# Kernel optimization log

Hardware: AMD Instinct MI355X
Metric: run time of the kernel (lower is better)

Reference implementation:

```python
import jax, jax.numpy as jnp
import numpy as np

LABEL_SMOOTHING = 0.1


def setup_inputs() -> dict:
    key = jax.random.key(0)
    k1, k2, k3 = jax.random.split(key, 3)
    B, N, D = 16384, 1000, 1000  # code structurally requires D == n_classes == N
    inputs = jax.random.uniform(k1, (B, D), dtype=jnp.float32)
    labels = jax.random.randint(k2, (B,), 0, N, dtype=jnp.int64)
    code_book = jax.random.uniform(k3, (N, D), dtype=jnp.float32)
    return {"inputs": inputs, "labels": labels, "code_book": code_book}


def reference(inputs, labels, code_book):
    # inputs: [B, D], code_book: [N, D], D == N (n_classes)
    n_classes = inputs.shape[1]
    # soft targets with label smoothing (same as scatter_ + smoothing)
    soft_target = jax.nn.one_hot(labels, n_classes, dtype=inputs.dtype)
    soft_target = soft_target * (1.0 - LABEL_SMOOTHING) + LABEL_SMOOTHING / n_classes
    # Hamming similarity: sum_d [o*c + (1-o)*(1-c)]  ==  o@c.T + (1-o)@(1-c).T
    # (algebraic rewrite of the [B, N, D] broadcast in the original; same math)
    similarity = (jnp.einsum("bd,nd->bn", inputs, code_book)
                  + jnp.einsum("bd,nd->bn", 1.0 - inputs, 1.0 - code_book))
    logp = jax.nn.log_softmax(similarity, axis=1)
    return jnp.mean(jnp.sum(-soft_target * logp, axis=1))
```

## Files before the change

### kernel.cpp

```cpp
#include <hip/hip_runtime.h>

typedef __attribute__((ext_vector_type(8))) short bf16x8;
typedef __attribute__((ext_vector_type(4))) float f32x4;

#define AS1 __attribute__((address_space(1)))
#define AS3 __attribute__((address_space(3)))

__device__ static inline void gl2lds16(const void* g, void* l) {
  __builtin_amdgcn_global_load_lds((const AS1 unsigned int*)g, (AS3 unsigned int*)l, 16, 0, 0);
}

__device__ static inline unsigned short f2bf(float x) {
  unsigned int u = __float_as_uint(x);
  unsigned int r = u + 0x7FFFu + ((u >> 16) & 1u);
  return (unsigned short)(r >> 16);
}

__global__ __launch_bounds__(256) void prep_all_k(
    const float* __restrict__ in, const int* __restrict__ labraw,
    const float* __restrict__ cb, unsigned short* __restrict__ a,
    unsigned short* __restrict__ b, float* __restrict__ rowsum,
    int* __restrict__ labs, float* __restrict__ lin, float* __restrict__ out) {
  const int bx = blockIdx.x, t = threadIdx.x;
  if (bx < 8192) {
    int idx = bx * 256 + t;
    int row = idx >> 7, g = idx & 127;
    union { unsigned short u[8]; uint4 v; } pk;
    if (g < 125) {
      const float4* p = (const float4*)(in + (size_t)row * 1000 + g * 8);
      float4 v0 = p[0], v1 = p[1];
      pk.u[0] = f2bf(2.f * v0.x); pk.u[1] = f2bf(2.f * v0.y);
      pk.u[2] = f2bf(2.f * v0.z); pk.u[3] = f2bf(2.f * v0.w);
      pk.u[4] = f2bf(2.f * v1.x); pk.u[5] = f2bf(2.f * v1.y);
      pk.u[6] = f2bf(2.f * v1.z); pk.u[7] = f2bf(2.f * v1.w);
    } else {
      pk.v = make_uint4(0, 0, 0, 0);
    }
    *(uint4*)(a + ((size_t)row << 10) + (g << 3)) = pk.v;
  } else if (bx < 9216) {
    int n = bx - 8192;
    float s = 0.f;
#pragma unroll
    for (int j = 0; j < 4; ++j) {
      int c = t + j * 256;
      float v = 0.f;
      if (n < 1000 && c < 1000) v = cb[(size_t)n * 1000 + c];
      s += v;
      b[((size_t)n << 10) + c] = f2bf(v);
    }
    __shared__ float red[256];
    red[t] = s;
    __syncthreads();
    for (int o = 128; o > 0; o >>= 1) {
      if (t < o) red[t] += red[t + o];
      __syncthreads();
    }
    if (t == 0) rowsum[n] = (n < 1000) ? red[0] : 0.f;
  } else {
    __shared__ int nz;
    if (t == 0) nz = 0;
    __syncthreads();
    if (labraw[2 * t + 1] != 0) atomicAdd(&nz, 1);
    __syncthreads();
    bool is64 = (nz < 32);
    int row = (bx - 9216) * 256 + t;
    labs[row] = is64 ? labraw[2 * row] : labraw[row];
    if (bx == 9216 && t == 0) { lin[0] = 0.f; out[0] = 0.f; }
  }
}

__global__ __launch_bounds__(512, 2) void coding_loss_k(
    const unsigned short* __restrict__ Ag,
    const unsigned short* __restrict__ Bg,
    const float* __restrict__ rowsum,
    const int* __restrict__ labels,
    float* __restrict__ Z,
    float* __restrict__ lin) {
  extern __shared__ __align__(16) unsigned short lds[];

  const int t    = threadIdx.x;
  const int lane = t & 63;
  const int w    = t >> 6;
  const int wr   = w >> 2;
  const int wc   = w & 3;
  const int g16  = lane >> 4;
  const int c16  = lane & 15;
  const int ct   = blockIdx.x & 3;
  const int rt   = blockIdx.x >> 2;
  const int r0   = rt << 8;
  const int c0   = ct << 8;

  size_t a_src[2], b_src[2]; int dstoff[2];
#pragma unroll
  for (int i = 0; i < 2; ++i) {
    int ch = i * 512 + t, row = ch >> 2;
    int sg = (ch & 3) ^ ((row >> 1) & 3);
    a_src[i] = (size_t)(r0 + row) * 1024 + sg * 8;
    b_src[i] = (size_t)(c0 + row) * 1024 + sg * 8;
    dstoff[i] = ch * 8;
  }
  int a_eoff[8], b_eoff[4];
#pragma unroll
  for (int i = 0; i < 8; ++i) {
    int ar = wr * 128 + i * 16 + c16;
    a_eoff[i] = ar * 32 + ((g16 ^ ((ar >> 1) & 3)) << 3);
  }
#pragma unroll
  for (int i = 0; i < 4; ++i) {
    int br = wc * 64 + i * 16 + c16;
    b_eoff[i] = br * 32 + ((g16 ^ ((br >> 1) & 3)) << 3);
  }

  f32x4 acc[8][4];
#pragma unroll
  for (int mi = 0; mi < 8; ++mi)
#pragma unroll
    for (int ni = 0; ni < 4; ++ni) acc[mi][ni] = (f32x4)(0.f);

#define TILE(J, DO_STAGE, DO_WAIT, WAIT_IMM)                                    \
  {                                                                             \
    unsigned short* pa = lds + ((J) & 3) * 8192;                                \
    unsigned short* pb = lds + 32768 + ((J) & 3) * 8192;                        \
    unsigned short* sa = lds + (((J) + 3) & 3) * 8192;                          \
    unsigned short* sb = lds + 32768 + (((J) + 3) & 3) * 8192;                  \
    if (DO_STAGE) {                                                             \
      _Pragma("unroll") for (int i = 0; i < 2; ++i)                             \
          gl2lds16(Ag + a_src[i] + ((J) + 3) * 32, sa + dstoff[i]);             \
      _Pragma("unroll") for (int i = 0; i < 2; ++i)                             \
          gl2lds16(Bg + b_src[i] + ((J) + 3) * 32, sb + dstoff[i]);             \
    }                                                                           \
    bf16x8 af[4], af2[4], bv[4];                                                \
    _Pragma("unroll") for (int i = 0; i < 4; ++i)                               \
        af[i] = *(const bf16x8*)(pa + a_eoff[i]);                               \
    _Pragma("unroll") for (int i = 0; i < 4; ++i)                               \
        bv[i] = *(const bf16x8*)(pb + b_eoff[i]);                               \
    _Pragma("unroll") for (int i = 0; i < 4; ++i)                               \
        af2[i] = *(const bf16x8*)(pa + a_eoff[i + 4]);                          \
    __builtin_amdgcn_s_setprio(1);                                              \
    _Pragma("unroll") for (int mi = 0; mi < 4; ++mi)                            \
      _Pragma("unroll") for (int ni = 0; ni < 4; ++ni)                          \
        acc[mi][ni] =                                                           \
            __builtin_amdgcn_mfma_f32_16x16x32_bf16(af[mi], bv[ni], acc[mi][ni], 0, 0, 0); \
    _Pragma("unroll") for (int mi = 0; mi < 4; ++mi)                            \
      _Pragma("unroll") for (int ni = 0; ni < 4; ++ni)                          \
        acc[mi + 4][ni] =                                                       \
            __builtin_amdgcn_mfma_f32_16x16x32_bf16(af2[mi], bv[ni], acc[mi + 4][ni], 0, 0, 0); \
    __builtin_amdgcn_s_setprio(0);                                              \
    if (DO_WAIT) __builtin_amdgcn_s_waitcnt(WAIT_IMM);                          \
    __builtin_amdgcn_s_barrier();                                               \
    __builtin_amdgcn_sched_barrier(0);                                          \
  }

#pragma unroll
  for (int q = 0; q < 3; ++q) {
#pragma unroll
    for (int i = 0; i < 2; ++i)
      gl2lds16(Ag + a_src[i] + q * 32, lds + q * 8192 + dstoff[i]);
#pragma unroll
    for (int i = 0; i < 2; ++i)
      gl2lds16(Bg + b_src[i] + q * 32, lds + 32768 + q * 8192 + dstoff[i]);
  }
  __builtin_amdgcn_s_waitcnt(0xF78);
  __builtin_amdgcn_s_barrier();
  __builtin_amdgcn_sched_barrier(0);

#pragma unroll 4
  for (int J = 0; J < 28; ++J) TILE(J, 1, 1, 0xF78);
  TILE(28, 1, 1, 0xF78);
  TILE(29, 0, 1, 0xF74);
  TILE(30, 0, 1, 0xF70);
  TILE(31, 0, 0, 0xF70);
#undef TILE
  __syncthreads();

  float* zbuf = (float*)lds;
  float* lbuf = zbuf + 1024;
  float rs[4]; int gcol[4];
#pragma unroll
  for (int ni = 0; ni < 4; ++ni) {
    gcol[ni] = c0 + wc * 64 + ni * 16 + c16;
    rs[ni]   = rowsum[gcol[ni]];
  }
  float lacc = 0.f;
#pragma unroll
  for (int mi = 0; mi < 8; ++mi) {
#pragma unroll
    for (int r = 0; r < 4; ++r) {
      int lrow = mi * 16 + g16 * 4 + r;
      int labv = labels[r0 + wr * 128 + lrow];
      float e = 0.f;
#pragma unroll
      for (int ni = 0; ni < 4; ++ni) {
        float S = acc[mi][ni][r] - rs[ni];
        e += __expf(S - 40.f);
        lacc += 1e-4f * S;
        if (gcol[ni] == labv) lacc += 0.9f * S;
      }
      e += __shfl_xor(e, 1, 64);
      e += __shfl_xor(e, 2, 64);
      e += __shfl_xor(e, 4, 64);
      e += __shfl_xor(e, 8, 64);
      if (c16 == 0) zbuf[w * 128 + lrow] = e;
    }
  }
#pragma unroll
  for (int d = 1; d < 64; d <<= 1) lacc += __shfl_xor(lacc, d, 64);
  if (lane == 0) lbuf[w] = lacc;
  __syncthreads();
  if (t < 256) {
    int wrg = t >> 7, l7 = t & 127;
    float z = zbuf[(wrg * 4 + 0) * 128 + l7] + zbuf[(wrg * 4 + 1) * 128 + l7] +
              zbuf[(wrg * 4 + 2) * 128 + l7] + zbuf[(wrg * 4 + 3) * 128 + l7];
    Z[ct * 16384 + r0 + t] = z;
  }
  if (t == 0)
    atomicAdd(lin, lbuf[0] + lbuf[1] + lbuf[2] + lbuf[3] +
                   lbuf[4] + lbuf[5] + lbuf[6] + lbuf[7]);
}

__global__ __launch_bounds__(256) void finalize_k(const float* __restrict__ Z,
                                                  const float* __restrict__ lin,
                                                  float* __restrict__ out) {
  int t = threadIdx.x;
  int row = blockIdx.x * 256 + t;
  float v = 40.f + logf(Z[row] + Z[16384 + row] + Z[2 * 16384 + row] + Z[3 * 16384 + row]);
#pragma unroll
  for (int d = 1; d < 64; d <<= 1) v += __shfl_xor(v, d, 64);
  __shared__ float s[4];
  if ((t & 63) == 0) s[t >> 6] = v;
  __syncthreads();
  if (t == 0) {
    float tot = s[0] + s[1] + s[2] + s[3];
    if (blockIdx.x == 0) tot -= lin[0];
    atomicAdd(out, tot * (1.f / 16384.f));
  }
}

extern "C" void kernel_launch(void* const* d_in, const int* in_sizes, int n_in,
                              void* d_out, int out_size, void* d_ws, size_t ws_size,
                              hipStream_t stream) {
  const float* inputs = (const float*)d_in[0];
  const int* labraw   = (const int*)d_in[1];
  const float* code   = (const float*)d_in[2];

  unsigned short* a_bf = (unsigned short*)d_ws;
  unsigned short* b_bf = a_bf + (size_t)16384 * 1024;
  float* rowsum        = (float*)(b_bf + (size_t)1024 * 1024);
  float* Z             = rowsum + 1024;
  float* lin           = Z + 4 * 16384;
  int* labs            = (int*)(lin + 1);

  static int lds_attr_set = 0;
  if (!lds_attr_set) {
    hipFuncSetAttribute(reinterpret_cast<const void*>(coding_loss_k),
                        hipFuncAttributeMaxDynamicSharedMemorySize, 131072);
    lds_attr_set = 1;
  }

  prep_all_k<<<9280, 256, 0, stream>>>(inputs, labraw, code, a_bf, b_bf, rowsum,
                                       labs, lin, (float*)d_out);
  coding_loss_k<<<256, 512, 131072, stream>>>(a_bf, b_bf, rowsum, labs, Z, lin);
  finalize_k<<<64, 256, 0, stream>>>(Z, lin, (float*)d_out);
}
```

Baseline: 140.5 us.

## Fuse fp32-to-bf16 input conversion into GEMM main loop with register staging

The separate prep pass that converted the 16384x1000 fp32 inputs to padded bf16 in workspace is removed. The GEMM kernel now loads fp32 rows straight from the inputs, converts them in registers and writes bf16 into a double-buffered static LDS tile. This drops a full write and reread of the converted A matrix. In exchange the previous 4-stage async global-to-LDS pipeline becomes a 2-stage register-prefetch pipeline with a full __syncthreads per tile, and each block reads twice as many bytes for A (fp32) and repeats the conversion work.

```diff
diff --git a/kernel.cpp b/kernel.cpp
--- a/kernel.cpp
+++ b/kernel.cpp
@@ -16,29 +16,13 @@
   return (unsigned short)(r >> 16);
 }
 
-__global__ __launch_bounds__(256) void prep_all_k(
-    const float* __restrict__ in, const int* __restrict__ labraw,
-    const float* __restrict__ cb, unsigned short* __restrict__ a,
+__global__ __launch_bounds__(256) void prep_bl_k(
+    const float* __restrict__ cb, const int* __restrict__ labraw,
     unsigned short* __restrict__ b, float* __restrict__ rowsum,
     int* __restrict__ labs, float* __restrict__ lin, float* __restrict__ out) {
   const int bx = blockIdx.x, t = threadIdx.x;
-  if (bx < 8192) {
-    int idx = bx * 256 + t;
-    int row = idx >> 7, g = idx & 127;
-    union { unsigned short u[8]; uint4 v; } pk;
-    if (g < 125) {
-      const float4* p = (const float4*)(in + (size_t)row * 1000 + g * 8);
-      float4 v0 = p[0], v1 = p[1];
-      pk.u[0] = f2bf(2.f * v0.x); pk.u[1] = f2bf(2.f * v0.y);
-      pk.u[2] = f2bf(2.f * v0.z); pk.u[3] = f2bf(2.f * v0.w);
-      pk.u[4] = f2bf(2.f * v1.x); pk.u[5] = f2bf(2.f * v1.y);
-      pk.u[6] = f2bf(2.f * v1.z); pk.u[7] = f2bf(2.f * v1.w);
-    } else {
-      pk.v = make_uint4(0, 0, 0, 0);
-    }
-    *(uint4*)(a + ((size_t)row << 10) + (g << 3)) = pk.v;
-  } else if (bx < 9216) {
-    int n = bx - 8192;
+  if (bx < 1024) {
+    int n = bx;
     float s = 0.f;
 #pragma unroll
     for (int j = 0; j < 4; ++j) {
@@ -63,20 +47,20 @@
     if (labraw[2 * t + 1] != 0) atomicAdd(&nz, 1);
     __syncthreads();
     bool is64 = (nz < 32);
-    int row = (bx - 9216) * 256 + t;
+    int row = (bx - 1024) * 256 + t;
     labs[row] = is64 ? labraw[2 * row] : labraw[row];
-    if (bx == 9216 && t == 0) { lin[0] = 0.f; out[0] = 0.f; }
+    if (bx == 1024 && t == 0) { lin[0] = 0.f; out[0] = 0.f; }
   }
 }
 
 __global__ __launch_bounds__(512, 2) void coding_loss_k(
-    const unsigned short* __restrict__ Ag,
+    const float* __restrict__ In,
     const unsigned short* __restrict__ Bg,
     const float* __restrict__ rowsum,
     const int* __restrict__ labels,
     float* __restrict__ Z,
     float* __restrict__ lin) {
-  extern __shared__ __align__(16) unsigned short lds[];
+  __shared__ __align__(16) unsigned short lds[32768];
 
   const int t    = threadIdx.x;
   const int lane = t & 63;
@@ -90,14 +74,17 @@
   const int r0   = rt << 8;
   const int c0   = ct << 8;
 
-  size_t a_src[2], b_src[2]; int dstoff[2];
+  const int sg  = (t & 3) ^ ((t >> 3) & 3);
+  const int rA0 = t >> 2, rA1 = 128 + (t >> 2);
+  const float* pA0 = In + (size_t)(r0 + rA0) * 1000 + sg * 8;
+  const float* pA1 = In + (size_t)(r0 + rA1) * 1000 + sg * 8;
+  size_t b_src[2]; int bdst[2];
 #pragma unroll
   for (int i = 0; i < 2; ++i) {
     int ch = i * 512 + t, row = ch >> 2;
-    int sg = (ch & 3) ^ ((row >> 1) & 3);
-    a_src[i] = (size_t)(r0 + row) * 1024 + sg * 8;
-    b_src[i] = (size_t)(c0 + row) * 1024 + sg * 8;
-    dstoff[i] = ch * 8;
+    int sgb = (ch & 3) ^ ((row >> 1) & 3);
+    b_src[i] = (size_t)(c0 + row) * 1024 + sgb * 8;
+    bdst[i] = ch * 8;
   }
   int a_eoff[8], b_eoff[4];
 #pragma unroll
@@ -117,60 +104,73 @@
 #pragma unroll
     for (int ni = 0; ni < 4; ++ni) acc[mi][ni] = (f32x4)(0.f);
 
-#define TILE(J, DO_STAGE, DO_WAIT, WAIT_IMM)                                    \
-  {                                                                             \
-    unsigned short* pa = lds + ((J) & 3) * 8192;                                \
-    unsigned short* pb = lds + 32768 + ((J) & 3) * 8192;                        \
-    unsigned short* sa = lds + (((J) + 3) & 3) * 8192;                          \
-    unsigned short* sb = lds + 32768 + (((J) + 3) & 3) * 8192;                  \
-    if (DO_STAGE) {                                                             \
-      _Pragma("unroll") for (int i = 0; i < 2; ++i)                             \
-          gl2lds16(Ag + a_src[i] + ((J) + 3) * 32, sa + dstoff[i]);             \
-      _Pragma("unroll") for (int i = 0; i < 2; ++i)                             \
-          gl2lds16(Bg + b_src[i] + ((J) + 3) * 32, sb + dstoff[i]);             \
-    }                                                                           \
-    bf16x8 af[4], af2[4], bv[4];                                                \
-    _Pragma("unroll") for (int i = 0; i < 4; ++i)                               \
-        af[i] = *(const bf16x8*)(pa + a_eoff[i]);                               \
-    _Pragma("unroll") for (int i = 0; i < 4; ++i)                               \
-        bv[i] = *(const bf16x8*)(pb + b_eoff[i]);                               \
-    _Pragma("unroll") for (int i = 0; i < 4; ++i)                               \
-        af2[i] = *(const bf16x8*)(pa + a_eoff[i + 4]);                          \
-    __builtin_amdgcn_s_setprio(1);                                              \
-    _Pragma("unroll") for (int mi = 0; mi < 4; ++mi)                            \
-      _Pragma("unroll") for (int ni = 0; ni < 4; ++ni)                          \
-        acc[mi][ni] =                                                           \
+#define LOADA(js, G0A, G0B, G1A, G1B)                                          \
+  {                                                                            \
+    if ((js) < 31 || sg == 0) {                                                \
+      const float4* q0 = (const float4*)(pA0 + (js) * 32);                     \
+      const float4* q1 = (const float4*)(pA1 + (js) * 32);                     \
+      G0A = q0[0]; G0B = q0[1]; G1A = q1[0]; G1B = q1[1];                      \
+    } else {                                                                   \
+      G0A = G0B = G1A = G1B = make_float4(0.f, 0.f, 0.f, 0.f);                 \
+    }                                                                          \
+  }
+
+#define CVWRA(p, G0A, G0B, G1A, G1B)                                           \
+  {                                                                            \
+    union { unsigned short u[8]; uint4 v; } w0, w1;                            \
+    w0.u[0] = f2bf(2.f * G0A.x); w0.u[1] = f2bf(2.f * G0A.y);                  \
+    w0.u[2] = f2bf(2.f * G0A.z); w0.u[3] = f2bf(2.f * G0A.w);                  \
+    w0.u[4] = f2bf(2.f * G0B.x); w0.u[5] = f2bf(2.f * G0B.y);                  \
+    w0.u[6] = f2bf(2.f * G0B.z); w0.u[7] = f2bf(2.f * G0B.w);                  \
+    w1.u[0] = f2bf(2.f * G1A.x); w1.u[1] = f2bf(2.f * G1A.y);                  \
+    w1.u[2] = f2bf(2.f * G1A.z); w1.u[3] = f2bf(2.f * G1A.w);                  \
+    w1.u[4] = f2bf(2.f * G1B.x); w1.u[5] = f2bf(2.f * G1B.y);                  \
+    w1.u[6] = f2bf(2.f * G1B.z); w1.u[7] = f2bf(2.f * G1B.w);                  \
+    *(uint4*)(lds + ((p) << 13) + t * 8) = w0.v;                               \
+    *(uint4*)(lds + ((p) << 13) + 4096 + t * 8) = w1.v;                        \
+  }
+
+#define COMPUTE(p)                                                             \
+  {                                                                            \
+    const unsigned short* pa = lds + ((p) << 13);                              \
+    const unsigned short* pb = lds + 16384 + ((p) << 13);                      \
+    bf16x8 af[4], af2[4], bv[4];                                               \
+    _Pragma("unroll") for (int i = 0; i < 4; ++i)                              \
+        af[i] = *(const bf16x8*)(pa + a_eoff[i]);                              \
+    _Pragma("unroll") for (int i = 0; i < 4; ++i)                              \
+        bv[i] = *(const bf16x8*)(pb + b_eoff[i]);                              \
+    _Pragma("unroll") for (int i = 0; i < 4; ++i)                              \
+        af2[i] = *(const bf16x8*)(pa + a_eoff[i + 4]);                         \
+    _Pragma("unroll") for (int mi = 0; mi < 4; ++mi)                           \
+      _Pragma("unroll") for (int ni = 0; ni < 4; ++ni)                         \
+        acc[mi][ni] =                                                          \
             __builtin_amdgcn_mfma_f32_16x16x32_bf16(af[mi], bv[ni], acc[mi][ni], 0, 0, 0); \
-    _Pragma("unroll") for (int mi = 0; mi < 4; ++mi)                            \
-      _Pragma("unroll") for (int ni = 0; ni < 4; ++ni)                          \
-        acc[mi + 4][ni] =                                                       \
+    _Pragma("unroll") for (int mi = 0; mi < 4; ++mi)                           \
+      _Pragma("unroll") for (int ni = 0; ni < 4; ++ni)                         \
+        acc[mi + 4][ni] =                                                      \
             __builtin_amdgcn_mfma_f32_16x16x32_bf16(af2[mi], bv[ni], acc[mi + 4][ni], 0, 0, 0); \
-    __builtin_amdgcn_s_setprio(0);                                              \
-    if (DO_WAIT) __builtin_amdgcn_s_waitcnt(WAIT_IMM);                          \
-    __builtin_amdgcn_s_barrier();                                               \
-    __builtin_amdgcn_sched_barrier(0);                                          \
-  }
-
-#pragma unroll
-  for (int q = 0; q < 3; ++q) {
-#pragma unroll
-    for (int i = 0; i < 2; ++i)
-      gl2lds16(Ag + a_src[i] + q * 32, lds + q * 8192 + dstoff[i]);
-#pragma unroll
-    for (int i = 0; i < 2; ++i)
-      gl2lds16(Bg + b_src[i] + q * 32, lds + 32768 + q * 8192 + dstoff[i]);
-  }
-  __builtin_amdgcn_s_waitcnt(0xF78);
-  __builtin_amdgcn_s_barrier();
-  __builtin_amdgcn_sched_barrier(0);
-
-#pragma unroll 4
-  for (int J = 0; J < 28; ++J) TILE(J, 1, 1, 0xF78);
-  TILE(28, 1, 1, 0xF78);
-  TILE(29, 0, 1, 0xF74);
-  TILE(30, 0, 1, 0xF70);
-  TILE(31, 0, 0, 0xF70);
-#undef TILE
+  }
+
+  {
+    float4 g0a, g0b, g1a, g1b;
+    LOADA(0, g0a, g0b, g1a, g1b);
+    gl2lds16(Bg + b_src[0], lds + 16384 + bdst[0]);
+    gl2lds16(Bg + b_src[1], lds + 16384 + bdst[1]);
+    CVWRA(0, g0a, g0b, g1a, g1b);
+    __syncthreads();
+  }
+
+  for (int J = 0; J < 31; ++J) {
+    const int jn = J + 1;
+    float4 g0a, g0b, g1a, g1b;
+    LOADA(jn, g0a, g0b, g1a, g1b);
+    gl2lds16(Bg + b_src[0] + jn * 32, lds + 16384 + ((jn & 1) << 13) + bdst[0]);
+    gl2lds16(Bg + b_src[1] + jn * 32, lds + 16384 + ((jn & 1) << 13) + bdst[1]);
+    COMPUTE(J & 1);
+    CVWRA(jn & 1, g0a, g0b, g1a, g1b);
+    __syncthreads();
+  }
+  COMPUTE(1);
   __syncthreads();
 
   float* zbuf = (float*)lds;
@@ -216,6 +216,9 @@
   if (t == 0)
     atomicAdd(lin, lbuf[0] + lbuf[1] + lbuf[2] + lbuf[3] +
                    lbuf[4] + lbuf[5] + lbuf[6] + lbuf[7]);
+#undef LOADA
+#undef CVWRA
+#undef COMPUTE
 }
 
 __global__ __launch_bounds__(256) void finalize_k(const float* __restrict__ Z,
@@ -243,22 +246,14 @@
   const int* labraw   = (const int*)d_in[1];
   const float* code   = (const float*)d_in[2];
 
-  unsigned short* a_bf = (unsigned short*)d_ws;
-  unsigned short* b_bf = a_bf + (size_t)16384 * 1024;
+  unsigned short* b_bf = (unsigned short*)d_ws;
   float* rowsum        = (float*)(b_bf + (size_t)1024 * 1024);
   float* Z             = rowsum + 1024;
   float* lin           = Z + 4 * 16384;
   int* labs            = (int*)(lin + 1);
 
-  static int lds_attr_set = 0;
-  if (!lds_attr_set) {
-    hipFuncSetAttribute(reinterpret_cast<const void*>(coding_loss_k),
-                        hipFuncAttributeMaxDynamicSharedMemorySize, 131072);
-    lds_attr_set = 1;
-  }
-
-  prep_all_k<<<9280, 256, 0, stream>>>(inputs, labraw, code, a_bf, b_bf, rowsum,
-                                       labs, lin, (float*)d_out);
-  coding_loss_k<<<256, 512, 131072, stream>>>(a_bf, b_bf, rowsum, labs, Z, lin);
+  prep_bl_k<<<1088, 256, 0, stream>>>(code, labraw, b_bf, rowsum, labs, lin,
+                                      (float*)d_out);
+  coding_loss_k<<<256, 512, 0, stream>>>(inputs, b_bf, rowsum, labs, Z, lin);
   finalize_k<<<64, 256, 0, stream>>>(Z, lin, (float*)d_out);
 }
```

New measurement: 166.9 us. 18.8% more time.

## Shrink GEMM block tile, use triple-buffered pipeline, fuse finalize via last-block reduction

Applied to the files above, without the earlier changes.

The GEMM kernel moves from 256x256 tiles with 512 threads and a 4-stage LDS ring to 128x256 tiles with 256 threads and a 3-stage ring. This doubles the grid to 512 blocks, and block IDs are remapped so neighbouring blocks are spread across XCDs. The separate finalize kernel is removed: a global counter lets the last block perform the logsumexp reduction and write the output, which saves a launch. In exchange, A-tile reuse per block is lower and the final reduction runs serially in a single block.

```diff
diff --git a/kernel.cpp b/kernel.cpp
--- a/kernel.cpp
+++ b/kernel.cpp
@@ -20,7 +20,8 @@
     const float* __restrict__ in, const int* __restrict__ labraw,
     const float* __restrict__ cb, unsigned short* __restrict__ a,
     unsigned short* __restrict__ b, float* __restrict__ rowsum,
-    int* __restrict__ labs, float* __restrict__ lin, float* __restrict__ out) {
+    int* __restrict__ labs, float* __restrict__ lin, float* __restrict__ out,
+    int* __restrict__ cnt) {
   const int bx = blockIdx.x, t = threadIdx.x;
   if (bx < 8192) {
     int idx = bx * 256 + t;
@@ -65,49 +66,56 @@
     bool is64 = (nz < 32);
     int row = (bx - 9216) * 256 + t;
     labs[row] = is64 ? labraw[2 * row] : labraw[row];
-    if (bx == 9216 && t == 0) { lin[0] = 0.f; out[0] = 0.f; }
-  }
-}
-
-__global__ __launch_bounds__(512, 2) void coding_loss_k(
+    if (bx == 9216 && t == 0) { lin[0] = 0.f; out[0] = 0.f; cnt[0] = 0; }
+  }
+}
+
+__global__ __launch_bounds__(256, 2) void coding_loss_k(
     const unsigned short* __restrict__ Ag,
     const unsigned short* __restrict__ Bg,
     const float* __restrict__ rowsum,
     const int* __restrict__ labels,
     float* __restrict__ Z,
-    float* __restrict__ lin) {
+    float* __restrict__ lin,
+    float* __restrict__ out,
+    int* __restrict__ cnt) {
   extern __shared__ __align__(16) unsigned short lds[];
 
   const int t    = threadIdx.x;
   const int lane = t & 63;
   const int w    = t >> 6;
-  const int wr   = w >> 2;
-  const int wc   = w & 3;
   const int g16  = lane >> 4;
   const int c16  = lane & 15;
-  const int ct   = blockIdx.x & 3;
-  const int rt   = blockIdx.x >> 2;
-  const int r0   = rt << 8;
+  const int bid  = blockIdx.x;
+  const int L    = ((bid & 7) << 6) | (bid >> 3);
+  const int ct   = L & 3;
+  const int rt   = L >> 2;
+  const int r0   = rt << 7;
   const int c0   = ct << 8;
 
-  size_t a_src[2], b_src[2]; int dstoff[2];
+  const int sg = (t & 3) ^ ((t >> 3) & 3);
+  const int rA = t >> 2;
+  size_t a_src[2]; int adst[2];
 #pragma unroll
   for (int i = 0; i < 2; ++i) {
-    int ch = i * 512 + t, row = ch >> 2;
-    int sg = (ch & 3) ^ ((row >> 1) & 3);
-    a_src[i] = (size_t)(r0 + row) * 1024 + sg * 8;
-    b_src[i] = (size_t)(c0 + row) * 1024 + sg * 8;
-    dstoff[i] = ch * 8;
+    a_src[i] = (size_t)(r0 + rA + 64 * i) * 1024 + sg * 8;
+    adst[i] = (t + 256 * i) * 8;
+  }
+  size_t b_src[4]; int bdst[4];
+#pragma unroll
+  for (int i = 0; i < 4; ++i) {
+    b_src[i] = (size_t)(c0 + rA + 64 * i) * 1024 + sg * 8;
+    bdst[i] = (t + 256 * i) * 8;
   }
   int a_eoff[8], b_eoff[4];
 #pragma unroll
   for (int i = 0; i < 8; ++i) {
-    int ar = wr * 128 + i * 16 + c16;
+    int ar = i * 16 + c16;
     a_eoff[i] = ar * 32 + ((g16 ^ ((ar >> 1) & 3)) << 3);
   }
 #pragma unroll
   for (int i = 0; i < 4; ++i) {
-    int br = wc * 64 + i * 16 + c16;
+    int br = w * 64 + i * 16 + c16;
     b_eoff[i] = br * 32 + ((g16 ^ ((br >> 1) & 3)) << 3);
   }
 
@@ -117,68 +125,74 @@
 #pragma unroll
     for (int ni = 0; ni < 4; ++ni) acc[mi][ni] = (f32x4)(0.f);
 
-#define TILE(J, DO_STAGE, DO_WAIT, WAIT_IMM)                                    \
-  {                                                                             \
-    unsigned short* pa = lds + ((J) & 3) * 8192;                                \
-    unsigned short* pb = lds + 32768 + ((J) & 3) * 8192;                        \
-    unsigned short* sa = lds + (((J) + 3) & 3) * 8192;                          \
-    unsigned short* sb = lds + 32768 + (((J) + 3) & 3) * 8192;                  \
-    if (DO_STAGE) {                                                             \
-      _Pragma("unroll") for (int i = 0; i < 2; ++i)                             \
-          gl2lds16(Ag + a_src[i] + ((J) + 3) * 32, sa + dstoff[i]);             \
-      _Pragma("unroll") for (int i = 0; i < 2; ++i)                             \
-          gl2lds16(Bg + b_src[i] + ((J) + 3) * 32, sb + dstoff[i]);             \
-    }                                                                           \
-    bf16x8 af[4], af2[4], bv[4];                                                \
-    _Pragma("unroll") for (int i = 0; i < 4; ++i)                               \
-        af[i] = *(const bf16x8*)(pa + a_eoff[i]);                               \
-    _Pragma("unroll") for (int i = 0; i < 4; ++i)                               \
-        bv[i] = *(const bf16x8*)(pb + b_eoff[i]);                               \
-    _Pragma("unroll") for (int i = 0; i < 4; ++i)                               \
-        af2[i] = *(const bf16x8*)(pa + a_eoff[i + 4]);                          \
-    __builtin_amdgcn_s_setprio(1);                                              \
-    _Pragma("unroll") for (int mi = 0; mi < 4; ++mi)                            \
-      _Pragma("unroll") for (int ni = 0; ni < 4; ++ni)                          \
-        acc[mi][ni] =                                                           \
+#define STAGE(js, qa, qb)                                                      \
+  {                                                                            \
+    _Pragma("unroll") for (int i = 0; i < 2; ++i)                              \
+        gl2lds16(Ag + a_src[i] + (size_t)(js) * 32, lds + (qa)*4096 + adst[i]); \
+    _Pragma("unroll") for (int i = 0; i < 4; ++i)                              \
+        gl2lds16(Bg + b_src[i] + (size_t)(js) * 32,                            \
+                 lds + 12288 + (qb)*8192 + bdst[i]);                           \
+  }
+
+#define COMPUTE(q)                                                             \
+  {                                                                            \
+    const unsigned short* pa = lds + (q)*4096;                                 \
+    const unsigned short* pb = lds + 12288 + (q)*8192;                         \
+    bf16x8 af[4], af2[4], bv[4];                                               \
+    _Pragma("unroll") for (int i = 0; i < 4; ++i)                              \
+        af[i] = *(const bf16x8*)(pa + a_eoff[i]);                              \
+    _Pragma("unroll") for (int i = 0; i < 4; ++i)                              \
+        bv[i] = *(const bf16x8*)(pb + b_eoff[i]);                              \
+    _Pragma("unroll") for (int i = 0; i < 4; ++i)                              \
+        af2[i] = *(const bf16x8*)(pa + a_eoff[i + 4]);                         \
+    _Pragma("unroll") for (int mi = 0; mi < 4; ++mi)                           \
+      _Pragma("unroll") for (int ni = 0; ni < 4; ++ni)                         \
+        acc[mi][ni] =                                                          \
             __builtin_amdgcn_mfma_f32_16x16x32_bf16(af[mi], bv[ni], acc[mi][ni], 0, 0, 0); \
-    _Pragma("unroll") for (int mi = 0; mi < 4; ++mi)                            \
-      _Pragma("unroll") for (int ni = 0; ni < 4; ++ni)                          \
-        acc[mi + 4][ni] =                                                       \
+    _Pragma("unroll") for (int mi = 0; mi < 4; ++mi)                           \
+      _Pragma("unroll") for (int ni = 0; ni < 4; ++ni)                         \
+        acc[mi + 4][ni] =                                                      \
             __builtin_amdgcn_mfma_f32_16x16x32_bf16(af2[mi], bv[ni], acc[mi + 4][ni], 0, 0, 0); \
-    __builtin_amdgcn_s_setprio(0);                                              \
-    if (DO_WAIT) __builtin_amdgcn_s_waitcnt(WAIT_IMM);                          \
-    __builtin_amdgcn_s_barrier();                                               \
-    __builtin_amdgcn_sched_barrier(0);                                          \
-  }
-
-#pragma unroll
-  for (int q = 0; q < 3; ++q) {
-#pragma unroll
-    for (int i = 0; i < 2; ++i)
-      gl2lds16(Ag + a_src[i] + q * 32, lds + q * 8192 + dstoff[i]);
-#pragma unroll
-    for (int i = 0; i < 2; ++i)
-      gl2lds16(Bg + b_src[i] + q * 32, lds + 32768 + q * 8192 + dstoff[i]);
-  }
-  __builtin_amdgcn_s_waitcnt(0xF78);
+  }
+
+#define REGION(q, js)                                                          \
+  {                                                                            \
+    STAGE(js, (q + 2) % 3, (q + 2) % 3);                                       \
+    COMPUTE(q);                                                                \
+    __builtin_amdgcn_sched_barrier(0);                                         \
+    __builtin_amdgcn_s_waitcnt(0xF76);                           \
+    __builtin_amdgcn_s_barrier();                                              \
+    __builtin_amdgcn_sched_barrier(0);                                         \
+  }
+
+  STAGE(0, 0, 0);
+  STAGE(1, 1, 1);
+  __builtin_amdgcn_s_waitcnt(0xF76);
   __builtin_amdgcn_s_barrier();
   __builtin_amdgcn_sched_barrier(0);
 
-#pragma unroll 4
-  for (int J = 0; J < 28; ++J) TILE(J, 1, 1, 0xF78);
-  TILE(28, 1, 1, 0xF78);
-  TILE(29, 0, 1, 0xF74);
-  TILE(30, 0, 1, 0xF70);
-  TILE(31, 0, 0, 0xF70);
-#undef TILE
+  for (int j0 = 0; j0 < 30; j0 += 3) {
+    REGION(0, j0 + 2);
+    REGION(1, j0 + 3);
+    REGION(2, j0 + 4);
+  }
+  COMPUTE(0);
+  __builtin_amdgcn_sched_barrier(0);
+  __builtin_amdgcn_s_waitcnt(0xF70);
+  __builtin_amdgcn_s_barrier();
+  __builtin_amdgcn_sched_barrier(0);
+  COMPUTE(1);
   __syncthreads();
+#undef STAGE
+#undef COMPUTE
+#undef REGION
 
   float* zbuf = (float*)lds;
-  float* lbuf = zbuf + 1024;
+  float* lbuf = zbuf + 512;
   float rs[4]; int gcol[4];
 #pragma unroll
   for (int ni = 0; ni < 4; ++ni) {
-    gcol[ni] = c0 + wc * 64 + ni * 16 + c16;
+    gcol[ni] = c0 + w * 64 + ni * 16 + c16;
     rs[ni]   = rowsum[gcol[ni]];
   }
   float lacc = 0.f;
@@ -187,7 +201,7 @@
 #pragma unroll
     for (int r = 0; r < 4; ++r) {
       int lrow = mi * 16 + g16 * 4 + r;
-      int labv = labels[r0 + wr * 128 + lrow];
+      int labv = labels[r0 + lrow];
       float e = 0.f;
 #pragma unroll
       for (int ni = 0; ni < 4; ++ni) {
@@ -207,32 +221,33 @@
   for (int d = 1; d < 64; d <<= 1) lacc += __shfl_xor(lacc, d, 64);
   if (lane == 0) lbuf[w] = lacc;
   __syncthreads();
-  if (t < 256) {
-    int wrg = t >> 7, l7 = t & 127;
-    float z = zbuf[(wrg * 4 + 0) * 128 + l7] + zbuf[(wrg * 4 + 1) * 128 + l7] +
-              zbuf[(wrg * 4 + 2) * 128 + l7] + zbuf[(wrg * 4 + 3) * 128 + l7];
-    Z[ct * 16384 + r0 + t] = z;
-  }
-  if (t == 0)
-    atomicAdd(lin, lbuf[0] + lbuf[1] + lbuf[2] + lbuf[3] +
-                   lbuf[4] + lbuf[5] + lbuf[6] + lbuf[7]);
-}
-
-__global__ __launch_bounds__(256) void finalize_k(const float* __restrict__ Z,
-                                                  const float* __restrict__ lin,
-                                                  float* __restrict__ out) {
-  int t = threadIdx.x;
-  int row = blockIdx.x * 256 + t;
-  float v = 40.f + logf(Z[row] + Z[16384 + row] + Z[2 * 16384 + row] + Z[3 * 16384 + row]);
-#pragma unroll
-  for (int d = 1; d < 64; d <<= 1) v += __shfl_xor(v, d, 64);
-  __shared__ float s[4];
-  if ((t & 63) == 0) s[t >> 6] = v;
+  if (t < 128) {
+    float z = zbuf[t] + zbuf[128 + t] + zbuf[256 + t] + zbuf[384 + t];
+    Z[(size_t)ct * 16384 + r0 + t] = z;
+  }
+  if (t == 0) atomicAdd(lin, lbuf[0] + lbuf[1] + lbuf[2] + lbuf[3]);
+
+  __threadfence();
+  __shared__ int amLast;
+  if (t == 0) amLast = (atomicAdd(cnt, 1) == (int)gridDim.x - 1);
   __syncthreads();
-  if (t == 0) {
-    float tot = s[0] + s[1] + s[2] + s[3];
-    if (blockIdx.x == 0) tot -= lin[0];
-    atomicAdd(out, tot * (1.f / 16384.f));
+  if (amLast) {
+    __threadfence();
+    float vsum = 0.f;
+    for (int row = t; row < 16384; row += 256) {
+      float zs = Z[row] + Z[16384 + row] + Z[2 * 16384 + row] + Z[3 * 16384 + row];
+      vsum += 40.f + logf(zs);
+    }
+#pragma unroll
+    for (int d = 1; d < 64; d <<= 1) vsum += __shfl_xor(vsum, d, 64);
+    float* fs = (float*)lds;
+    __syncthreads();
+    if (lane == 0) fs[w] = vsum;
+    __syncthreads();
+    if (t == 0) {
+      float tot = fs[0] + fs[1] + fs[2] + fs[3] - lin[0];
+      out[0] = tot * (1.f / 16384.f);
+    }
   }
 }
 
@@ -249,16 +264,17 @@
   float* Z             = rowsum + 1024;
   float* lin           = Z + 4 * 16384;
   int* labs            = (int*)(lin + 1);
+  int* cnt             = labs + 16384;
 
   static int lds_attr_set = 0;
   if (!lds_attr_set) {
     hipFuncSetAttribute(reinterpret_cast<const void*>(coding_loss_k),
-                        hipFuncAttributeMaxDynamicSharedMemorySize, 131072);
+                        hipFuncAttributeMaxDynamicSharedMemorySize, 73728);
     lds_attr_set = 1;
   }
 
   prep_all_k<<<9280, 256, 0, stream>>>(inputs, labraw, code, a_bf, b_bf, rowsum,
-                                       labs, lin, (float*)d_out);
-  coding_loss_k<<<256, 512, 131072, stream>>>(a_bf, b_bf, rowsum, labs, Z, lin);
-  finalize_k<<<64, 256, 0, stream>>>(Z, lin, (float*)d_out);
-}
+                                       labs, lin, (float*)d_out, cnt);
+  coding_loss_k<<<512, 256, 73728, stream>>>(a_bf, b_bf, rowsum, labs, Z, lin,
+                                             (float*)d_out, cnt);
+}
```

New measurement: 189.9 us. +35.2%, slower.
